# Performance work log

Hardware: AMD Instinct MI355X
Metric: run time of the kernel (lower is better)

## Reference

```python
import jax, jax.numpy as jnp
import numpy as np

B, N, C = 4, 4096, 512
C8 = C // 8

def setup_inputs() -> dict:
    key = jax.random.key(0)
    ks = jax.random.split(key, 4)
    x = jax.random.normal(ks[0], (B, N, C), dtype=jnp.float32)
    # 1x1 Conv1D kernels == dense matmuls over channel dim
    Wf = jax.random.normal(ks[1], (C, C8), dtype=jnp.float32) * 0.02
    bf = jnp.zeros((C8,), dtype=jnp.float32)
    Wg = jax.random.normal(ks[2], (C, C8), dtype=jnp.float32) * 0.02
    bg = jnp.zeros((C8,), dtype=jnp.float32)
    Wh = jax.random.normal(ks[3], (C, C), dtype=jnp.float32) * 0.02
    bh = jnp.zeros((C,), dtype=jnp.float32)
    gamma = jnp.float32(1.0)  # learned scalar (zero-init in original; nonzero to exercise path)
    return {"x": x, "Wf": Wf, "bf": bf, "Wg": Wg, "bg": bg, "Wh": Wh, "bh": bh, "gamma": gamma}

def reference(x, Wf, bf, Wg, bg, Wh, bh, gamma):
    # 1x1 conv projections (kernel_size=1 -> per-position matmul)
    f_x = jnp.einsum('bnc,cd->bnd', x, Wf) + bf          # [B, N, C/8]
    g_x = jnp.einsum('bnc,cd->bnd', x, Wg) + bg          # [B, N, C/8]
    h_x = jnp.einsum('bnc,cd->bnd', x, Wh) + bh          # [B, N, C]
    # unscaled single-head attention: softmax(f g^T) h
    scores = jnp.einsum('bnd,bmd->bnm', f_x, g_x)        # [B, N, N]
    attn = jax.nn.softmax(scores, axis=-1)
    out = jnp.einsum('bnm,bmd->bnd', attn, h_x)          # [B, N, C]
    return x + gamma * out
```

## Files before the change

kernel.cpp:

```cpp
#include <hip/hip_runtime.h>
#include <stdint.h>

typedef uint16_t u16;
typedef __attribute__((ext_vector_type(8)))  __bf16    bf16x8;
typedef __attribute__((ext_vector_type(4)))  __bf16    bf16x4;
typedef __attribute__((ext_vector_type(8)))  uint16_t  u16x8;
typedef __attribute__((ext_vector_type(4)))  uint16_t  u16x4;
typedef __attribute__((ext_vector_type(4)))  float     f32x4;

#define LOG2E 1.44269504088896340736f
#define MFMA16(a, b, c) __builtin_amdgcn_mfma_f32_16x16x32_bf16((a), (b), (c), 0, 0, 0)

__device__ __forceinline__ u16 f2b(float f) {
  uint32_t u = __builtin_bit_cast(uint32_t, f);
  u += 0x7fffu + ((u >> 16) & 1u);
  return (u16)(u >> 16);
}

__device__ __forceinline__ bf16x8 ldsFrag(const u16* base, int row, int chunk) {
  const u16* p = base + row * 64 + ((chunk ^ (row & 7)) << 3);
  u16x8 raw = *(const u16x8*)p;
  return __builtin_bit_cast(bf16x8, raw);
}
__device__ __forceinline__ void ldsPut(u16* base, int row, int logicalChunk, u16x8 v) {
  u16* p = base + row * 64 + ((logicalChunk ^ (row & 7)) << 3);
  *(u16x8*)p = v;
}

__device__ __forceinline__ void dma16(const u16* g, u16* l) {
  __builtin_amdgcn_global_load_lds(
      (const __attribute__((address_space(1))) uint32_t*)g,
      (__attribute__((address_space(3))) uint32_t*)l, 16, 0, 0);
}

__global__ __launch_bounds__(256) void xconv(
    const float* __restrict__ x, u16* __restrict__ xb) {
  size_t idx = ((size_t)blockIdx.x * 256 + threadIdx.x) * 8;
  f32x4 a0 = *(const f32x4*)(x + idx);
  f32x4 a1 = *(const f32x4*)(x + idx + 4);
  u16x8 v;
#pragma unroll
  for (int i = 0; i < 4; ++i) { v[i] = f2b(a0[i]); v[4 + i] = f2b(a1[i]); }
  *(u16x8*)(xb + idx) = v;
}

__global__ __launch_bounds__(256) void pack_weights2(
    const float* __restrict__ Wf, const float* __restrict__ Wg,
    const float* __restrict__ Wh, const float* __restrict__ bfv,
    const float* __restrict__ bgv, const float* __restrict__ bhv,
    u16* __restrict__ Wt, float* __restrict__ biasc) {
  __shared__ u16 T[64 * 64];
  const int nt = blockIdx.x >> 3;
  const int kt = blockIdx.x & 7;
  const int n0 = nt * 64, k0 = kt * 64;
  const float* src; int stride, cbase; float scale = 1.0f;
  if (nt == 0)      { src = Wf; stride = 64;  cbase = 0;        scale = LOG2E; }
  else if (nt == 1) { src = Wg; stride = 64;  cbase = 0; }
  else              { src = Wh; stride = 512; cbase = n0 - 128; }
  const int t = threadIdx.x;
  const int cl = (t & 15) * 4, r0 = t >> 4;
#pragma unroll
  for (int j = 0; j < 4; ++j) {
    int r = r0 + j * 16;
    f32x4 v = *(const f32x4*)(src + (size_t)(k0 + r) * stride + cbase + cl);
    u16x4 o;
#pragma unroll
    for (int i = 0; i < 4; ++i) o[i] = f2b(v[i] * scale);
    *(u16x4*)(T + r * 64 + cl) = o;
  }
  __syncthreads();
  const int n = t >> 2, kq = (t & 3) * 16;
  u16x8 a, b2;
#pragma unroll
  for (int i = 0; i < 8; ++i) { a[i] = T[(kq + i) * 64 + n]; b2[i] = T[(kq + 8 + i) * 64 + n]; }
  *(u16x8*)(Wt + (size_t)(n0 + n) * 512 + k0 + kq) = a;
  *(u16x8*)(Wt + (size_t)(n0 + n) * 512 + k0 + kq + 8) = b2;
  if (kt == 0 && t < 64) {
    float bv = (nt == 0) ? bfv[t] * LOG2E : (nt == 1) ? bgv[t] : bhv[cbase + t];
    biasc[n0 + t] = bv;
  }
}

__global__ __launch_bounds__(256, 2) void proj_gemm(
    const u16* __restrict__ xb, const u16* __restrict__ Wt,
    const float* __restrict__ biasc,
    u16* __restrict__ fo, u16* __restrict__ go, u16* __restrict__ ht) {
  __shared__ u16 smem[128 * 128];
  u16* lds_a = smem;
  u16* lds_b = smem + 128 * 64;
  const int t = threadIdx.x, lane = t & 63, wave = t >> 6;
  const int m0 = blockIdx.x * 128, n0 = blockIdx.y * 128;
  const int wr = wave >> 1, wc = wave & 1;
  const int l15 = lane & 15, l4 = lane >> 4;
  const int dmarow = lane >> 3, dmachunk = (lane & 7) ^ (lane >> 3);

  f32x4 acc[4][4];
#pragma unroll
  for (int i = 0; i < 4; ++i)
#pragma unroll
    for (int j = 0; j < 4; ++j) acc[i][j] = (f32x4)(0.f);

  for (int kb = 0; kb < 8; ++kb) {
    const int k0 = kb * 64;
    if (kb) __syncthreads();
#pragma unroll
    for (int ii = 0; ii < 4; ++ii) {
      int rw = wave * 32 + ii * 8;
      dma16(xb + (size_t)(m0 + rw + dmarow) * 512 + k0 + dmachunk * 8,
            lds_a + rw * 64);
    }
#pragma unroll
    for (int ii = 0; ii < 4; ++ii) {
      int rw = wave * 32 + ii * 8;
      dma16(Wt + (size_t)(n0 + rw + dmarow) * 512 + k0 + dmachunk * 8,
            lds_b + rw * 64);
    }
    __syncthreads();
#pragma unroll
    for (int ks = 0; ks < 2; ++ks) {
      const int chunk = ks * 4 + l4;
      bf16x8 af[4], bq[4];
#pragma unroll
      for (int mt = 0; mt < 4; ++mt) af[mt] = ldsFrag(lds_a, wr * 64 + mt * 16 + l15, chunk);
#pragma unroll
      for (int nt = 0; nt < 4; ++nt) bq[nt] = ldsFrag(lds_b, wc * 64 + nt * 16 + l15, chunk);
#pragma unroll
      for (int mt = 0; mt < 4; ++mt)
#pragma unroll
        for (int nt = 0; nt < 4; ++nt) acc[mt][nt] = MFMA16(af[mt], bq[nt], acc[mt][nt]);
    }
  }

  if (n0 >= 128) {
    __syncthreads();
#pragma unroll
    for (int nt = 0; nt < 4; ++nt) {
      int nl = wc * 64 + nt * 16 + l15;
      float bv = biasc[n0 + nl];
#pragma unroll
      for (int mt = 0; mt < 4; ++mt) {
        int mb = wr * 64 + mt * 16 + (l4 << 2);
        f32x4 a = acc[mt][nt];
        u16x4 v;
#pragma unroll
        for (int r = 0; r < 4; ++r) v[r] = f2b(a[r] + bv);
        u16* dst = smem + nl * 128 + (((mb >> 3) ^ (nl & 7)) << 3) + (mb & 7);
        *(u16x4*)dst = v;
      }
    }
    __syncthreads();
    const int bb = m0 >> 12, posb = m0 & 4095;
    const int row0 = t >> 4, c16 = t & 15;
#pragma unroll
    for (int j = 0; j < 8; ++j) {
      int rr = row0 + j * 16;
      u16x8 v = *(const u16x8*)(smem + rr * 128 + ((c16 ^ (rr & 7)) << 3));
      int vcol = n0 - 128 + rr;
      *(u16x8*)(ht + ((size_t)(bb * 512 + vcol) << 12) + posb + c16 * 8) = v;
    }
  } else {
#pragma unroll
    for (int nt = 0; nt < 4; ++nt) {
      int n = wc * 64 + nt * 16 + l15;
      float bv = biasc[n];
#pragma unroll
      for (int mt = 0; mt < 4; ++mt) {
        int mrow = m0 + wr * 64 + mt * 16 + (l4 << 2);
        f32x4 a = acc[mt][nt];
        if (n < 64) {
#pragma unroll
          for (int r = 0; r < 4; ++r) fo[(size_t)(mrow + r) * 64 + n] = f2b(a[r] + bv);
        } else {
#pragma unroll
          for (int r = 0; r < 4; ++r) go[(size_t)(mrow + r) * 64 + (n - 64)] = f2b(a[r] + bv);
        }
      }
    }
  }
}

__global__ __launch_bounds__(256, 4) void attn3(
    const u16* __restrict__ fq, const u16* __restrict__ gk,
    const u16* __restrict__ ht, const float* __restrict__ x,
    const float* __restrict__ gamma_p, float* __restrict__ out) {
  __shared__ u16 lds_g[64 * 64];
  __shared__ u16 lds_p[64 * 64];
  __shared__ float lds_red[4 * 64];
  __shared__ float lds_linv[64];

  const int i = blockIdx.x;
  const int slice = i & 15;
  const int b = slice >> 2, vq = slice & 3;
  const int qb = i >> 4;
  const int q0 = qb * 64, vc0 = vq * 128;

  const int t = threadIdx.x, lane = t & 63, w = t >> 6;
  const int l15 = lane & 15, l4 = lane >> 4;
  const float gamma = gamma_p[0];
  const int dmarow = lane >> 3, dmachunk = (lane & 7) ^ (lane >> 3);

  const u16* gkb = gk + (size_t)(b * 4096) * 64;
  const u16* htw = ht + ((size_t)(b * 512 + vc0 + w * 32)) * 4096;

  bf16x8 fB[4][2];
#pragma unroll
  for (int qt = 0; qt < 4; ++qt)
#pragma unroll
    for (int ks = 0; ks < 2; ++ks) {
      const u16* p = fq + (size_t)(b * 4096 + q0 + qt * 16 + l15) * 64 + ks * 32 + l4 * 8;
      fB[qt][ks] = __builtin_bit_cast(bf16x8, *(const u16x8*)p);
    }

  f32x4 oacc[4][2];
#pragma unroll
  for (int qt = 0; qt < 4; ++qt)
#pragma unroll
    for (int ct = 0; ct < 2; ++ct) oacc[qt][ct] = (f32x4)(0.f);
  float lrun[4] = {0.f, 0.f, 0.f, 0.f};

  auto stage_g = [&](int k0g) {
#pragma unroll
    for (int ii = 0; ii < 2; ++ii) {
      int rw = w * 16 + ii * 8;
      const u16* src = gkb + (size_t)(k0g + rw + dmarow) * 64 + dmachunk * 8;
      dma16(src, lds_g + rw * 64);
    }
  };

  stage_g(0);
  __syncthreads();

  for (int kt = 0; kt < 64; ++kt) {
    const int k0 = kt * 64;
    f32x4 sacc[4];
#pragma unroll
    for (int qt = 0; qt < 4; ++qt) sacc[qt] = (f32x4)(0.f);
#pragma unroll
    for (int ks = 0; ks < 2; ++ks) {
      bf16x8 gA = ldsFrag(lds_g, w * 16 + l15, ks * 4 + l4);
#pragma unroll
      for (int qt = 0; qt < 4; ++qt) sacc[qt] = MFMA16(gA, fB[qt][ks], sacc[qt]);
    }
#pragma unroll
    for (int qt = 0; qt < 4; ++qt) {
      f32x4 s = sacc[qt];
      f32x4 p;
#pragma unroll
      for (int r = 0; r < 4; ++r) p[r] = __builtin_amdgcn_exp2f(s[r]);
      lrun[qt] += (p[0] + p[1]) + (p[2] + p[3]);
      bf16x4 pb;
#pragma unroll
      for (int r = 0; r < 4; ++r) pb[r] = (__bf16)p[r];
      int row = qt * 16 + l15;
      int keyb = w * 16 + (l4 << 2);
      u16* dst = lds_p + row * 64 + (((keyb >> 3) ^ (row & 7)) << 3) + (keyb & 7);
      *(u16x4*)dst = __builtin_bit_cast(u16x4, pb);
    }
    __syncthreads();
    if (kt < 63) stage_g(k0 + 64);
#pragma unroll
    for (int ks = 0; ks < 2; ++ks) {
      bf16x8 hb[2], pf[4];
#pragma unroll
      for (int ct = 0; ct < 2; ++ct) {
        const u16* hp = htw + (size_t)(ct * 16 + l15) * 4096 + k0 + ks * 32 + l4 * 8;
        hb[ct] = __builtin_bit_cast(bf16x8, *(const u16x8*)hp);
      }
#pragma unroll
      for (int qt = 0; qt < 4; ++qt)
        pf[qt] = ldsFrag(lds_p, qt * 16 + l15, ks * 4 + l4);
#pragma unroll
      for (int qt = 0; qt < 4; ++qt)
#pragma unroll
        for (int ct = 0; ct < 2; ++ct)
          oacc[qt][ct] = MFMA16(pf[qt], hb[ct], oacc[qt][ct]);
    }
    __syncthreads();
  }

#pragma unroll
  for (int qt = 0; qt < 4; ++qt) {
    lrun[qt] += __shfl_xor(lrun[qt], 16);
    lrun[qt] += __shfl_xor(lrun[qt], 32);
  }
  if (l4 == 0) {
#pragma unroll
    for (int qt = 0; qt < 4; ++qt) lds_red[w * 64 + qt * 16 + l15] = lrun[qt];
  }
  __syncthreads();
  if (t < 64) {
    float s = (lds_red[t] + lds_red[64 + t]) + (lds_red[128 + t] + lds_red[192 + t]);
    lds_linv[t] = 1.0f / s;
  }
  __syncthreads();

#pragma unroll
  for (int qt = 0; qt < 4; ++qt) {
    f32x4 linv = *(const f32x4*)&lds_linv[qt * 16 + (l4 << 2)];
#pragma unroll
    for (int ct = 0; ct < 2; ++ct) {
      int c = vc0 + w * 32 + ct * 16 + l15;
#pragma unroll
      for (int r = 0; r < 4; ++r) {
        int q = q0 + qt * 16 + (l4 << 2) + r;
        size_t idx = ((size_t)(b * 4096 + q) << 9) + c;
        out[idx] = x[idx] + gamma * oacc[qt][ct][r] * linv[r];
      }
    }
  }
}

extern "C" void kernel_launch(void* const* d_in, const int* in_sizes, int n_in,
                              void* d_out, int out_size, void* d_ws, size_t ws_size,
                              hipStream_t stream) {
  const float* x   = (const float*)d_in[0];
  const float* Wf  = (const float*)d_in[1];
  const float* bfv = (const float*)d_in[2];
  const float* Wg  = (const float*)d_in[3];
  const float* bgv = (const float*)d_in[4];
  const float* Wh  = (const float*)d_in[5];
  const float* bhv = (const float*)d_in[6];
  const float* gam = (const float*)d_in[7];
  float* out = (float*)d_out;

  char* ws = (char*)d_ws;
  u16*   Wt    = (u16*)(ws);
  float* biasc = (float*)(ws + 655360);
  u16*   fo    = (u16*)(ws + 657920);
  u16*   go    = (u16*)(ws + 2755072);
  u16*   ht    = (u16*)(ws + 4852224);
  u16*   xb    = (u16*)(ws + 21629440);

  xconv<<<4096, 256, 0, stream>>>(x, xb);
  pack_weights2<<<80, 256, 0, stream>>>(Wf, Wg, Wh, bfv, bgv, bhv, Wt, biasc);
  proj_gemm<<<dim3(128, 5), 256, 0, stream>>>(xb, Wt, biasc, fo, go, ht);
  attn3<<<1024, 256, 0, stream>>>(fo, go, ht, x, gam, out);
}
```

Baseline: 248.7 us.

## Double query tile per block to share G staging and H loads across 128 queries

The attention kernel now uses 512-thread blocks covering 128 queries instead of 64. Two wave groups each compute scores for half the queries against a shared 64-key G tile. All 8 waves then reuse the combined P tile, each wave handling 16 value channels for all 128 queries. This halves per-query G staging and H global reads and the block count, in exchange for a larger LDS footprint, more LDS P reads per wave, and fewer blocks (512) to fill the GPU.

```diff
diff --git a/kernel.cpp b/kernel.cpp
--- a/kernel.cpp
+++ b/kernel.cpp
@@ -179,52 +179,47 @@
   }
 }
 
-__global__ __launch_bounds__(256, 4) void attn3(
+__global__ __launch_bounds__(512, 4) void attn12(
     const u16* __restrict__ fq, const u16* __restrict__ gk,
     const u16* __restrict__ ht, const float* __restrict__ x,
     const float* __restrict__ gamma_p, float* __restrict__ out) {
   __shared__ u16 lds_g[64 * 64];
-  __shared__ u16 lds_p[64 * 64];
-  __shared__ float lds_red[4 * 64];
-  __shared__ float lds_linv[64];
+  __shared__ u16 lds_p[128 * 64];
+  __shared__ float lds_red[8 * 64];
+  __shared__ float lds_linv[128];
 
   const int i = blockIdx.x;
   const int slice = i & 15;
   const int b = slice >> 2, vq = slice & 3;
   const int qb = i >> 4;
-  const int q0 = qb * 64, vc0 = vq * 128;
+  const int q0 = qb * 128, vc0 = vq * 128;
 
   const int t = threadIdx.x, lane = t & 63, w = t >> 6;
   const int l15 = lane & 15, l4 = lane >> 4;
+  const int h = w >> 2, kq = w & 3;
   const float gamma = gamma_p[0];
   const int dmarow = lane >> 3, dmachunk = (lane & 7) ^ (lane >> 3);
 
   const u16* gkb = gk + (size_t)(b * 4096) * 64;
-  const u16* htw = ht + ((size_t)(b * 512 + vc0 + w * 32)) * 4096;
+  const u16* htw = ht + ((size_t)(b * 512 + vc0 + w * 16)) * 4096;
 
   bf16x8 fB[4][2];
 #pragma unroll
   for (int qt = 0; qt < 4; ++qt)
 #pragma unroll
     for (int ks = 0; ks < 2; ++ks) {
-      const u16* p = fq + (size_t)(b * 4096 + q0 + qt * 16 + l15) * 64 + ks * 32 + l4 * 8;
+      const u16* p = fq + (size_t)(b * 4096 + q0 + h * 64 + qt * 16 + l15) * 64 + ks * 32 + l4 * 8;
       fB[qt][ks] = __builtin_bit_cast(bf16x8, *(const u16x8*)p);
     }
 
-  f32x4 oacc[4][2];
-#pragma unroll
-  for (int qt = 0; qt < 4; ++qt)
-#pragma unroll
-    for (int ct = 0; ct < 2; ++ct) oacc[qt][ct] = (f32x4)(0.f);
+  f32x4 oacc[8];
+#pragma unroll
+  for (int qt = 0; qt < 8; ++qt) oacc[qt] = (f32x4)(0.f);
   float lrun[4] = {0.f, 0.f, 0.f, 0.f};
 
   auto stage_g = [&](int k0g) {
-#pragma unroll
-    for (int ii = 0; ii < 2; ++ii) {
-      int rw = w * 16 + ii * 8;
-      const u16* src = gkb + (size_t)(k0g + rw + dmarow) * 64 + dmachunk * 8;
-      dma16(src, lds_g + rw * 64);
-    }
+    const u16* src = gkb + (size_t)(k0g + w * 8 + dmarow) * 64 + dmachunk * 8;
+    dma16(src, lds_g + (w * 8) * 64);
   };
 
   stage_g(0);
@@ -237,7 +232,7 @@
     for (int qt = 0; qt < 4; ++qt) sacc[qt] = (f32x4)(0.f);
 #pragma unroll
     for (int ks = 0; ks < 2; ++ks) {
-      bf16x8 gA = ldsFrag(lds_g, w * 16 + l15, ks * 4 + l4);
+      bf16x8 gA = ldsFrag(lds_g, kq * 16 + l15, ks * 4 + l4);
 #pragma unroll
       for (int qt = 0; qt < 4; ++qt) sacc[qt] = MFMA16(gA, fB[qt][ks], sacc[qt]);
     }
@@ -251,8 +246,8 @@
       bf16x4 pb;
 #pragma unroll
       for (int r = 0; r < 4; ++r) pb[r] = (__bf16)p[r];
-      int row = qt * 16 + l15;
-      int keyb = w * 16 + (l4 << 2);
+      int row = h * 64 + qt * 16 + l15;
+      int keyb = kq * 16 + (l4 << 2);
       u16* dst = lds_p + row * 64 + (((keyb >> 3) ^ (row & 7)) << 3) + (keyb & 7);
       *(u16x4*)dst = __builtin_bit_cast(u16x4, pb);
     }
@@ -260,20 +255,13 @@
     if (kt < 63) stage_g(k0 + 64);
 #pragma unroll
     for (int ks = 0; ks < 2; ++ks) {
-      bf16x8 hb[2], pf[4];
-#pragma unroll
-      for (int ct = 0; ct < 2; ++ct) {
-        const u16* hp = htw + (size_t)(ct * 16 + l15) * 4096 + k0 + ks * 32 + l4 * 8;
-        hb[ct] = __builtin_bit_cast(bf16x8, *(const u16x8*)hp);
+      const u16* hp = htw + (size_t)l15 * 4096 + k0 + ks * 32 + l4 * 8;
+      bf16x8 hb = __builtin_bit_cast(bf16x8, *(const u16x8*)hp);
+#pragma unroll
+      for (int qt = 0; qt < 8; ++qt) {
+        bf16x8 pf = ldsFrag(lds_p, qt * 16 + l15, ks * 4 + l4);
+        oacc[qt] = MFMA16(pf, hb, oacc[qt]);
       }
-#pragma unroll
-      for (int qt = 0; qt < 4; ++qt)
-        pf[qt] = ldsFrag(lds_p, qt * 16 + l15, ks * 4 + l4);
-#pragma unroll
-      for (int qt = 0; qt < 4; ++qt)
-#pragma unroll
-        for (int ct = 0; ct < 2; ++ct)
-          oacc[qt][ct] = MFMA16(pf[qt], hb[ct], oacc[qt][ct]);
     }
     __syncthreads();
   }
@@ -288,24 +276,23 @@
     for (int qt = 0; qt < 4; ++qt) lds_red[w * 64 + qt * 16 + l15] = lrun[qt];
   }
   __syncthreads();
-  if (t < 64) {
-    float s = (lds_red[t] + lds_red[64 + t]) + (lds_red[128 + t] + lds_red[192 + t]);
+  if (t < 128) {
+    int hh = t >> 6, ql = t & 63;
+    float s = (lds_red[(hh * 4 + 0) * 64 + ql] + lds_red[(hh * 4 + 1) * 64 + ql]) +
+              (lds_red[(hh * 4 + 2) * 64 + ql] + lds_red[(hh * 4 + 3) * 64 + ql]);
     lds_linv[t] = 1.0f / s;
   }
   __syncthreads();
 
 #pragma unroll
-  for (int qt = 0; qt < 4; ++qt) {
+  for (int qt = 0; qt < 8; ++qt) {
     f32x4 linv = *(const f32x4*)&lds_linv[qt * 16 + (l4 << 2)];
-#pragma unroll
-    for (int ct = 0; ct < 2; ++ct) {
-      int c = vc0 + w * 32 + ct * 16 + l15;
-#pragma unroll
-      for (int r = 0; r < 4; ++r) {
-        int q = q0 + qt * 16 + (l4 << 2) + r;
-        size_t idx = ((size_t)(b * 4096 + q) << 9) + c;
-        out[idx] = x[idx] + gamma * oacc[qt][ct][r] * linv[r];
-      }
+    int c = vc0 + w * 16 + l15;
+#pragma unroll
+    for (int r = 0; r < 4; ++r) {
+      int q = q0 + qt * 16 + (l4 << 2) + r;
+      size_t idx = ((size_t)(b * 4096 + q) << 9) + c;
+      out[idx] = x[idx] + gamma * oacc[qt][r] * linv[r];
     }
   }
 }
@@ -334,5 +321,5 @@
   xconv<<<4096, 256, 0, stream>>>(x, xb);
   pack_weights2<<<80, 256, 0, stream>>>(Wf, Wg, Wh, bfv, bgv, bhv, Wt, biasc);
   proj_gemm<<<dim3(128, 5), 256, 0, stream>>>(xb, Wt, biasc, fo, go, ht);
-  attn3<<<1024, 256, 0, stream>>>(fo, go, ht, x, gam, out);
-}
+  attn12<<<512, 512, 0, stream>>>(fo, go, ht, x, gam, out);
+}
```

New measurement: 219.1 us. 11.9% less time.
